# Kernel optimization log

Hardware: AMD Instinct MI355X
Metric: run time of the kernel (lower is better)

Reference implementation:

```python
import jax, jax.numpy as jnp
import numpy as np

N_NODES = 100000
N_EDGES = 800000
N_LAYERS = 6
GATE_TYPES = 29
H = 256        # hidden dim
INTER = 256    # inter dim
EDGE_F = 3     # (src_idx, dst_idx, reversed) edge features


def setup_inputs() -> dict:
    key = jax.random.key(0)
    ks = jax.random.split(key, 16)
    gate_type = jax.random.randint(ks[0], (N_NODES,), 0, GATE_TYPES)
    src = jax.random.randint(ks[1], (N_EDGES,), 0, N_NODES)
    dst = jax.random.randint(ks[2], (N_EDGES,), 0, N_NODES)
    w = jax.random.uniform(ks[3], (N_EDGES, EDGE_F), dtype=jnp.float32)
    s = 0.05
    emb = jax.random.normal(ks[4], (GATE_TYPES, H), dtype=jnp.float32) * s
    # QConv per layer: linear1 (no bias): [INTER, H+3]; linear2: [H, H+INTER] + bias
    W1 = jax.random.normal(ks[5], (N_LAYERS, INTER, H + EDGE_F), dtype=jnp.float32) * s
    W2 = jax.random.normal(ks[6], (N_LAYERS, H, H + INTER), dtype=jnp.float32) * s
    b2 = jax.random.normal(ks[7], (N_LAYERS, H), dtype=jnp.float32) * s
    # MLP head 256->256->1
    Wh1 = jax.random.normal(ks[8], (H, H), dtype=jnp.float32) * s
    bh1 = jax.random.normal(ks[9], (H,), dtype=jnp.float32) * s
    Wh2 = jax.random.normal(ks[10], (1, H), dtype=jnp.float32) * s
    bh2 = jax.random.normal(ks[11], (1,), dtype=jnp.float32) * s
    return {"gate_type": gate_type, "src": src, "dst": dst, "w": w,
            "emb": emb, "W1": W1, "W2": W2, "b2": b2,
            "Wh1": Wh1, "bh1": bh1, "Wh2": Wh2, "bh2": bh2}


def reference(gate_type, src, dst, w, emb, W1, W2, b2, Wh1, bh1, Wh2, bh2):
    n = gate_type.shape[0]
    h = emb[gate_type]                                   # [N, H]
    deg = jax.ops.segment_sum(jnp.ones((src.shape[0],), h.dtype), dst, num_segments=n)
    inv_deg = (1.0 / jnp.maximum(deg, 1.0))[:, None]      # mean over mailbox; 0-deg nodes -> h_N = 0
    for l in range(W1.shape[0]):
        m = jnp.concatenate([h[src], w], axis=1)          # [E, H+3] gather
        tmp = jax.nn.leaky_relu(m @ W1[l].T, 0.01)        # [E, INTER]
        h_N = jax.ops.segment_sum(tmp, dst, num_segments=n) * inv_deg  # scatter-mean [N, INTER]
        h = jax.nn.relu(jnp.concatenate([h, h_N], axis=1) @ W2[l].T + b2[l])
    x = jax.nn.relu(h @ Wh1.T + bh1)                      # [N, H]
    return x @ Wh2.T + bh2                                # [N, 1]
```

## Files before the change

### kernel.cpp

```cpp
#include <hip/hip_runtime.h>

#define H 256
#define NLAYERS 6
typedef unsigned int uint32;
typedef unsigned short u16;

typedef __bf16 bf16;
typedef bf16 bf16x8 __attribute__((ext_vector_type(8)));
typedef float f32x4 __attribute__((ext_vector_type(4)));
typedef u16 u16x8 __attribute__((ext_vector_type(8)));

__device__ __forceinline__ float bf2f(u16 h) {
    return __uint_as_float(((uint32)h) << 16);
}
__device__ __forceinline__ u16 f2bf(float f) {
    uint32 u = __float_as_uint(f);
    u = u + 0x7FFFu + ((u >> 16) & 1u);
    return (u16)(u >> 16);
}

__device__ __forceinline__ void glds16(const void* src, const char* ldsdst) {
    __builtin_amdgcn_global_load_lds(
        (const __attribute__((address_space(1))) void*)src,
        (__attribute__((address_space(3))) void*)ldsdst, 16, 0, 0);
}


__global__ __launch_bounds__(256)
void count_kernel(const int* __restrict__ dst, int* __restrict__ deg, int E) {
    int e = blockIdx.x * 256 + threadIdx.x;
    if (e < E) atomicAdd(&deg[dst[e]], 1);
}

__global__ __launch_bounds__(256)
void invd_kernel(const int* __restrict__ deg, float* __restrict__ invd, int N) {
    int n = blockIdx.x * 256 + threadIdx.x;
    if (n < N) invd[n] = 1.f / fmaxf((float)deg[n], 1.f);
}

__global__ __launch_bounds__(256)
void scan1_kernel(const int* __restrict__ deg, int* __restrict__ bsum, int N) {
    __shared__ int s[256];
    int t = threadIdx.x;
    int i = blockIdx.x * 256 + t;
    s[t] = (i < N) ? deg[i] : 0;
    __syncthreads();
    for (int off = 128; off; off >>= 1) {
        if (t < off) s[t] += s[t + off];
        __syncthreads();
    }
    if (t == 0) bsum[blockIdx.x] = s[0];
}

__global__ __launch_bounds__(512)
void scan2_kernel(int* __restrict__ bsum, int nb) {
    __shared__ int s[512];
    int t = threadIdx.x;
    int v = (t < nb) ? bsum[t] : 0;
    s[t] = v;
    __syncthreads();
    for (int off = 1; off < 512; off <<= 1) {
        int x = (t >= off) ? s[t - off] : 0;
        __syncthreads();
        s[t] += x;
        __syncthreads();
    }
    if (t < nb) bsum[t] = s[t] - v;
}

__global__ __launch_bounds__(256)
void scan3_kernel(const int* __restrict__ deg, const int* __restrict__ bsum,
                  int* __restrict__ rowptr, int N, int E) {
    __shared__ int s[256];
    int t = threadIdx.x;
    int i = blockIdx.x * 256 + t;
    int v = (i < N) ? deg[i] : 0;
    s[t] = v;
    __syncthreads();
    for (int off = 1; off < 256; off <<= 1) {
        int x = (t >= off) ? s[t - off] : 0;
        __syncthreads();
        s[t] += x;
        __syncthreads();
    }
    if (i < N) rowptr[i] = s[t] - v + bsum[blockIdx.x];
    if (i == 0) rowptr[N] = E;
}

__global__ __launch_bounds__(256)
void scatter_kernel(const int* __restrict__ src, const int* __restrict__ dst,
                    const float* __restrict__ w, const int* __restrict__ rowptr,
                    int* __restrict__ cursor, int* __restrict__ srcS,
                    float* __restrict__ wS, int E) {
    int e = blockIdx.x * 256 + threadIdx.x;
    if (e >= E) return;
    int d = dst[e];
    int p = rowptr[d] + atomicAdd(&cursor[d], 1);
    srcS[p] = src[e];
    float4 wq;
    wq.x = w[(size_t)e * 3 + 0];
    wq.y = w[(size_t)e * 3 + 1];
    wq.z = w[(size_t)e * 3 + 2];
    wq.w = 0.f;
    *(float4*)&wS[(size_t)p * 4] = wq;
}


__global__ __launch_bounds__(256)
void wsplit_kernel(const float* __restrict__ W1, const float* __restrict__ W2,
                   const float* __restrict__ Wh1,
                   u16* __restrict__ W1hi, u16* __restrict__ W1lo,
                   u16* __restrict__ W2hi, u16* __restrict__ W2lo,
                   u16* __restrict__ Wh1hi, u16* __restrict__ Wh1lo)
{
    int i = blockIdx.x * 256 + threadIdx.x;
    float v; u16* ph; u16* pl; int o;
    if (i < 393216) {
        int l = i >> 16, rem = i & 65535, r = rem >> 8, k = rem & 255;
        v = W1[(size_t)l * 66304 + (size_t)r * 259 + k];
        ph = W1hi; pl = W1lo; o = i;
    } else if (i < 1179648) {
        int j = i - 393216;
        v = W2[j];
        ph = W2hi; pl = W2lo; o = j;
    } else if (i < 1245184) {
        int j = i - 1179648;
        v = Wh1[j];
        ph = Wh1hi; pl = Wh1lo; o = j;
    } else return;
    u16 hi = f2bf(v);
    ph[o] = hi;
    pl[o] = f2bf(v - bf2f(hi));
}

__global__ void extract_kernel(const float* __restrict__ W1, float* __restrict__ ccAll)
{
    int l = blockIdx.x;
    int i = threadIdx.x;
    const float* W1l = W1 + (size_t)l * 66304;
    float* cc = ccAll + (size_t)l * 768;
    #pragma unroll
    for (int j = 0; j < 3; ++j)
        cc[j * 256 + i] = W1l[(size_t)i * 259 + 256 + j];
}


__global__ __launch_bounds__(256)
void emb_split_kernel(const int* __restrict__ gt, const float* __restrict__ emb,
                      u16* __restrict__ hHi, u16* __restrict__ hLo, int N) {
    size_t idx = (size_t)blockIdx.x * 256 + threadIdx.x;
    if (idx >= (size_t)N * 256) return;
    int n = (int)(idx >> 8), c = (int)(idx & 255);
    float v = emb[(size_t)gt[n] * 256 + c];
    u16 hi = f2bf(v);
    hHi[idx] = hi;
    hLo[idx] = f2bf(v - bf2f(hi));
}


#define LDS_AHI 0
#define LDS_ALO 4096
#define LDS_WHI 8192
#define LDS_WLO 24576

template<bool MAIN>
__device__ __forceinline__ void do_compute(const char* lds, const int* aoff,
                                           const int* woff, f32x4 (&acc)[4][4]) {
    bf16x8 ah[4], al[4];
    #pragma unroll
    for (int mi = 0; mi < 4; ++mi) {
        ah[mi] = *(const bf16x8*)(lds + LDS_AHI + aoff[mi]);
        if (MAIN) al[mi] = *(const bf16x8*)(lds + LDS_ALO + aoff[mi]);
    }
    #pragma unroll
    for (int nj = 0; nj < 4; ++nj) {
        bf16x8 wh = *(const bf16x8*)(lds + LDS_WHI + woff[nj]);
        bf16x8 wl = *(const bf16x8*)(lds + LDS_WLO + woff[nj]);
        #pragma unroll
        for (int mi = 0; mi < 4; ++mi) {
            acc[mi][nj] = __builtin_amdgcn_mfma_f32_16x16x32_bf16(wh, ah[mi], acc[mi][nj], 0, 0, 0);
            acc[mi][nj] = __builtin_amdgcn_mfma_f32_16x16x32_bf16(wl, ah[mi], acc[mi][nj], 0, 0, 0);
            if (MAIN)
                acc[mi][nj] = __builtin_amdgcn_mfma_f32_16x16x32_bf16(wh, al[mi], acc[mi][nj], 0, 0, 0);
        }
    }
}

template<int KTOT, bool BIASRELU, bool WLO>
__global__ __launch_bounds__(256)
void mfma_gemm_kernel(const u16* __restrict__ Ahi_, const u16* __restrict__ Alo_,
                      const u16* __restrict__ A2_,
                      const u16* __restrict__ Whi_, const u16* __restrict__ Wlo_,
                      const float* __restrict__ bias,
                      u16* __restrict__ Chi, u16* __restrict__ Clo, int M)
{
    __shared__ __align__(128) char lds[40960];
    const int tid = threadIdx.x;
    const int wv = tid >> 6;
    const int lane = tid & 63;
    const int m0 = blockIdx.x * 64;
    const int lrow = lane & 15, koct = lane >> 4;

    int aoff[4], woff[4];
    #pragma unroll
    for (int mi = 0; mi < 4; ++mi) {
        int r = mi * 16 + lrow;
        aoff[mi] = r * 64 + ((koct ^ (r & 3)) << 4);
    }
    #pragma unroll
    for (int nj = 0; nj < 4; ++nj) {
        int r = wv * 64 + nj * 16 + lrow;
        woff[nj] = r * 64 + ((koct ^ (r & 3)) << 4);
    }

    const int arow = tid >> 2;
    const int acs = (tid & 3) ^ (arow & 3);
    const long agrow = (long)((m0 + arow < M) ? (m0 + arow) : (M - 1));
    const char* Asrc_hi = (const char*)Ahi_ + agrow * 512 + acs * 16;
    const char* Asrc_lo = (const char*)Alo_ + agrow * 512 + acs * 16;
    const char* Asrc_2  = (const char*)A2_  + agrow * 512 + acs * 16;

    f32x4 acc[4][4] = {};

    for (int k0 = 0; k0 < 256; k0 += 32) {
        glds16(Asrc_hi + k0 * 2, lds + LDS_AHI + wv * 1024);
        glds16(Asrc_lo + k0 * 2, lds + LDS_ALO + wv * 1024);
        #pragma unroll
        for (int rr = 0; rr < 4; ++rr) {
            int f = rr * 256 + tid;
            int wr = f >> 2;
            int wcs = (f & 3) ^ (wr & 3);
            glds16((const char*)Whi_ + (long)wr * (KTOT * 2) + k0 * 2 + wcs * 16,
                   lds + LDS_WHI + rr * 4096 + wv * 1024);
            glds16((const char*)Wlo_ + (long)wr * (KTOT * 2) + k0 * 2 + wcs * 16,
                   lds + LDS_WLO + rr * 4096 + wv * 1024);
        }
        __syncthreads();
        do_compute<true>(lds, aoff, woff, acc);
        __syncthreads();
    }
    if (KTOT > 256) {
        for (int k0 = 256; k0 < KTOT; k0 += 32) {
            glds16(Asrc_2 + (k0 - 256) * 2, lds + LDS_AHI + wv * 1024);
            #pragma unroll
            for (int rr = 0; rr < 4; ++rr) {
                int f = rr * 256 + tid;
                int wr = f >> 2;
                int wcs = (f & 3) ^ (wr & 3);
                glds16((const char*)Whi_ + (long)wr * (KTOT * 2) + k0 * 2 + wcs * 16,
                       lds + LDS_WHI + rr * 4096 + wv * 1024);
                glds16((const char*)Wlo_ + (long)wr * (KTOT * 2) + k0 * 2 + wcs * 16,
                       lds + LDS_WLO + rr * 4096 + wv * 1024);
            }
            __syncthreads();
            do_compute<false>(lds, aoff, woff, acc);
            __syncthreads();
        }
    }

    float4 bv[4];
    if (BIASRELU) {
        #pragma unroll
        for (int nj = 0; nj < 4; ++nj)
            bv[nj] = *(const float4*)&bias[wv * 64 + nj * 16 + koct * 4];
    }
    #pragma unroll
    for (int mi = 0; mi < 4; ++mi) {
        int row = m0 + mi * 16 + lrow;
        if (row >= M) continue;
        #pragma unroll
        for (int nj = 0; nj < 4; ++nj) {
            f32x4 v = acc[mi][nj];
            if (BIASRELU) {
                v[0] = fmaxf(v[0] + bv[nj].x, 0.f);
                v[1] = fmaxf(v[1] + bv[nj].y, 0.f);
                v[2] = fmaxf(v[2] + bv[nj].z, 0.f);
                v[3] = fmaxf(v[3] + bv[nj].w, 0.f);
            }
            size_t o = (size_t)row * 256 + wv * 64 + nj * 16 + koct * 4;
            ushort4 ohi;
            ohi.x = f2bf(v[0]); ohi.y = f2bf(v[1]);
            ohi.z = f2bf(v[2]); ohi.w = f2bf(v[3]);
            *(ushort4*)&Chi[o] = ohi;
            if (WLO) {
                ushort4 olo;
                olo.x = f2bf(v[0] - bf2f(ohi.x));
                olo.y = f2bf(v[1] - bf2f(ohi.y));
                olo.z = f2bf(v[2] - bf2f(ohi.z));
                olo.w = f2bf(v[3] - bf2f(ohi.w));
                *(ushort4*)&Clo[o] = olo;
            }
        }
    }
}


__global__ __launch_bounds__(256)
void edge_agg_kernel(const int* __restrict__ rowptr, const int* __restrict__ srcS,
                     const float* __restrict__ wS, const u16* __restrict__ T,
                     const float* __restrict__ cc, const float* __restrict__ invd,
                     u16* __restrict__ hN, int N) {
    int n = blockIdx.x * 4 + (threadIdx.x >> 6);
    int lane = threadIdx.x & 63;
    if (n >= N) return;
    const int half = lane >> 5;
    const int c32 = lane & 31;
    const int col0 = c32 * 8;

    float c0[8], c1[8], c2[8];
    #pragma unroll
    for (int j = 0; j < 3; ++j) {
        float4 lo4 = *(const float4*)&cc[j * 256 + col0];
        float4 hi4 = *(const float4*)&cc[j * 256 + col0 + 4];
        float* cj = (j == 0) ? c0 : (j == 1) ? c1 : c2;
        cj[0] = lo4.x; cj[1] = lo4.y; cj[2] = lo4.z; cj[3] = lo4.w;
        cj[4] = hi4.x; cj[5] = hi4.y; cj[6] = hi4.z; cj[7] = hi4.w;
    }

    float acc[8] = {};
    const int e0 = rowptr[n], e1 = rowptr[n + 1];
    int e = e0 + half;
    for (; e + 2 < e1; e += 4) {
        int s0 = srcS[e];
        int s1 = srcS[e + 2];
        float4 wa = *(const float4*)&wS[(size_t)e * 4];
        float4 wb = *(const float4*)&wS[(size_t)(e + 2) * 4];
        u16x8 t0 = *(const u16x8*)&T[(size_t)s0 * 256 + col0];
        u16x8 t1 = *(const u16x8*)&T[(size_t)s1 * 256 + col0];
        #pragma unroll
        for (int q = 0; q < 8; ++q) {
            float x = fmaf(wa.x, c0[q], fmaf(wa.y, c1[q], fmaf(wa.z, c2[q], bf2f(t0[q]))));
            acc[q] += (x > 0.f) ? x : 0.01f * x;
            float y = fmaf(wb.x, c0[q], fmaf(wb.y, c1[q], fmaf(wb.z, c2[q], bf2f(t1[q]))));
            acc[q] += (y > 0.f) ? y : 0.01f * y;
        }
    }
    for (; e < e1; e += 2) {
        int s0 = srcS[e];
        float4 wa = *(const float4*)&wS[(size_t)e * 4];
        u16x8 t0 = *(const u16x8*)&T[(size_t)s0 * 256 + col0];
        #pragma unroll
        for (int q = 0; q < 8; ++q) {
            float x = fmaf(wa.x, c0[q], fmaf(wa.y, c1[q], fmaf(wa.z, c2[q], bf2f(t0[q]))));
            acc[q] += (x > 0.f) ? x : 0.01f * x;
        }
    }
    #pragma unroll
    for (int q = 0; q < 8; ++q) acc[q] += __shfl_xor(acc[q], 32);
    if (half == 0) {
        float sc = invd[n];
        u16x8 o;
        #pragma unroll
        for (int q = 0; q < 8; ++q) o[q] = f2bf(acc[q] * sc);
        *(u16x8*)&hN[(size_t)n * 256 + col0] = o;
    }
}


__global__ __launch_bounds__(256)
void head_out_kernel(const u16* __restrict__ xhi, const u16* __restrict__ xlo,
                     const float* __restrict__ wh2,
                     const float* __restrict__ bh2, float* __restrict__ out, int N) {
    int n = blockIdx.x * 4 + (threadIdx.x >> 6);
    int lane = threadIdx.x & 63;
    if (n >= N) return;
    ushort4 hv = ((const ushort4*)(xhi + (size_t)n * H))[lane];
    ushort4 lv = ((const ushort4*)(xlo + (size_t)n * H))[lane];
    float4 wv = ((const float4*)wh2)[lane];
    float x0 = bf2f(hv.x) + bf2f(lv.x);
    float x1 = bf2f(hv.y) + bf2f(lv.y);
    float x2 = bf2f(hv.z) + bf2f(lv.z);
    float x3 = bf2f(hv.w) + bf2f(lv.w);
    float sum = x0 * wv.x + x1 * wv.y + x2 * wv.z + x3 * wv.w;
    #pragma unroll
    for (int off = 32; off; off >>= 1) sum += __shfl_xor(sum, off);
    if (lane == 0) out[n] = sum + bh2[0];
}


extern "C" void kernel_launch(void* const* d_in, const int* in_sizes, int n_in,
                              void* d_out, int out_size, void* d_ws, size_t ws_size,
                              hipStream_t stream) {
    const int*   gate_type = (const int*)d_in[0];
    const int*   src  = (const int*)d_in[1];
    const int*   dst  = (const int*)d_in[2];
    const float* w    = (const float*)d_in[3];
    const float* emb  = (const float*)d_in[4];
    const float* W1   = (const float*)d_in[5];
    const float* W2   = (const float*)d_in[6];
    const float* b2   = (const float*)d_in[7];
    const float* Wh1  = (const float*)d_in[8];
    const float* bh1  = (const float*)d_in[9];
    const float* Wh2  = (const float*)d_in[10];
    const float* bh2  = (const float*)d_in[11];
    float* out = (float*)d_out;

    const int N = in_sizes[0];
    const int E = in_sizes[1];

    char* p = (char*)d_ws;
    auto alloc = [&](size_t bytes) -> char* {
        char* r = p;
        p += (bytes + 1023) & ~(size_t)1023;
        return r;
    };
    u16*   hHi   = (u16*)  alloc((size_t)N * H * 2);
    u16*   hLo   = (u16*)  alloc((size_t)N * H * 2);
    u16*   tBuf  = (u16*)  alloc((size_t)N * H * 2);
    u16*   hNBuf = (u16*)  alloc((size_t)N * H * 2);
    int*   srcS  = (int*)  alloc((size_t)E * 4);
    float* wS    = (float*)alloc((size_t)E * 4 * 4);
    int*   rowptr= (int*)  alloc((size_t)(N + 1) * 4);
    int*   cursor= (int*)  alloc((size_t)N * 4);
    int*   bsum  = (int*)  alloc(4096);
    float* invd  = (float*)alloc((size_t)N * 4);
    float* ccAll = (float*)alloc(6u * 768 * 4);
    u16*   W1hi  = (u16*)  alloc(6u * 256 * 256 * 2);
    u16*   W1lo  = (u16*)  alloc(6u * 256 * 256 * 2);
    u16*   W2hi  = (u16*)  alloc(6u * 256 * 512 * 2);
    u16*   W2lo  = (u16*)  alloc(6u * 256 * 512 * 2);
    u16*   Wh1hi = (u16*)  alloc(256u * 256 * 2);
    u16*   Wh1lo = (u16*)  alloc(256u * 256 * 2);

    const int nb1 = (N + 255) / 256;

    hipMemsetAsync(cursor, 0, (size_t)N * 4, stream);
    count_kernel<<<(E + 255) / 256, 256, 0, stream>>>(dst, cursor, E);
    invd_kernel<<<nb1, 256, 0, stream>>>(cursor, invd, N);
    scan1_kernel<<<nb1, 256, 0, stream>>>(cursor, bsum, N);
    scan2_kernel<<<1, 512, 0, stream>>>(bsum, nb1);
    scan3_kernel<<<nb1, 256, 0, stream>>>(cursor, bsum, rowptr, N, E);
    hipMemsetAsync(cursor, 0, (size_t)N * 4, stream);
    scatter_kernel<<<(E + 255) / 256, 256, 0, stream>>>(src, dst, w, rowptr, cursor, srcS, wS, E);

    wsplit_kernel<<<4864, 256, 0, stream>>>(W1, W2, Wh1, W1hi, W1lo, W2hi, W2lo, Wh1hi, Wh1lo);
    extract_kernel<<<6, 256, 0, stream>>>(W1, ccAll);
    emb_split_kernel<<<N, 256, 0, stream>>>(gate_type, emb, hHi, hLo, N);

    const int gm = (N + 63) / 64;
    for (int l = 0; l < NLAYERS; ++l) {
        mfma_gemm_kernel<256, false, false><<<gm, 256, 0, stream>>>(
            hHi, hLo, nullptr, W1hi + (size_t)l * 65536, W1lo + (size_t)l * 65536,
            nullptr, tBuf, nullptr, N);
        edge_agg_kernel<<<(N + 3) / 4, 256, 0, stream>>>(
            rowptr, srcS, wS, tBuf, ccAll + (size_t)l * 768, invd, hNBuf, N);
        mfma_gemm_kernel<512, true, true><<<gm, 256, 0, stream>>>(
            hHi, hLo, hNBuf, W2hi + (size_t)l * 131072, W2lo + (size_t)l * 131072,
            b2 + (size_t)l * 256, hHi, hLo, N);
    }
    mfma_gemm_kernel<256, true, true><<<gm, 256, 0, stream>>>(
        hHi, hLo, nullptr, Wh1hi, Wh1lo, bh1, hHi, hLo, N);
    head_out_kernel<<<(N + 3) / 4, 256, 0, stream>>>(hHi, hLo, Wh2, bh2, out, N);
}
```

Before: 1.885 ms.

## Enlarge GEMM tile to 128 rows with 8 waves, unroll edge gather by 4

The MFMA GEMM now processes 128 rows per block with 512 threads arranged as 2 row-halves by 4 column groups. This halves the number of times each weight tile is reloaded into LDS per node, and the weight source pointers are precomputed outside the k-loop. The LDS swizzle is changed to use (row>>1)&3. In the edge aggregation kernel the loop is unrolled to four gathers per iteration to put more loads in flight. The cost is more LDS per block (48KB), a larger block that may lower occupancy, and more register pressure in the edge kernel.

```diff
diff --git a/kernel.cpp b/kernel.cpp
--- a/kernel.cpp
+++ b/kernel.cpp
@@ -159,9 +159,9 @@
 
 
 #define LDS_AHI 0
-#define LDS_ALO 4096
-#define LDS_WHI 8192
-#define LDS_WLO 24576
+#define LDS_ALO 8192
+#define LDS_WHI 16384
+#define LDS_WLO 32768
 
 template<bool MAIN>
 __device__ __forceinline__ void do_compute(const char* lds, const int* aoff,
@@ -187,54 +187,56 @@
 }
 
 template<int KTOT, bool BIASRELU, bool WLO>
-__global__ __launch_bounds__(256)
+__global__ __launch_bounds__(512)
 void mfma_gemm_kernel(const u16* __restrict__ Ahi_, const u16* __restrict__ Alo_,
                       const u16* __restrict__ A2_,
                       const u16* __restrict__ Whi_, const u16* __restrict__ Wlo_,
                       const float* __restrict__ bias,
                       u16* __restrict__ Chi, u16* __restrict__ Clo, int M)
 {
-    __shared__ __align__(128) char lds[40960];
+    __shared__ __align__(128) char lds[49152];
     const int tid = threadIdx.x;
     const int wv = tid >> 6;
     const int lane = tid & 63;
-    const int m0 = blockIdx.x * 64;
+    const int m0 = blockIdx.x * 128;
     const int lrow = lane & 15, koct = lane >> 4;
+    const int rh = wv & 1, cg = wv >> 1;
 
     int aoff[4], woff[4];
     #pragma unroll
     for (int mi = 0; mi < 4; ++mi) {
-        int r = mi * 16 + lrow;
-        aoff[mi] = r * 64 + ((koct ^ (r & 3)) << 4);
+        int r = rh * 64 + mi * 16 + lrow;
+        aoff[mi] = r * 64 + ((koct ^ ((r >> 1) & 3)) << 4);
     }
     #pragma unroll
     for (int nj = 0; nj < 4; ++nj) {
-        int r = wv * 64 + nj * 16 + lrow;
-        woff[nj] = r * 64 + ((koct ^ (r & 3)) << 4);
+        int r = cg * 64 + nj * 16 + lrow;
+        woff[nj] = r * 64 + ((koct ^ ((r >> 1) & 3)) << 4);
     }
 
     const int arow = tid >> 2;
-    const int acs = (tid & 3) ^ (arow & 3);
+    const int achk = (tid & 3) ^ ((arow >> 1) & 3);
     const long agrow = (long)((m0 + arow < M) ? (m0 + arow) : (M - 1));
-    const char* Asrc_hi = (const char*)Ahi_ + agrow * 512 + acs * 16;
-    const char* Asrc_lo = (const char*)Alo_ + agrow * 512 + acs * 16;
-    const char* Asrc_2  = (const char*)A2_  + agrow * 512 + acs * 16;
+    const char* Asrc_hi = (const char*)Ahi_ + agrow * 512 + achk * 16;
+    const char* Asrc_lo = (const char*)Alo_ + agrow * 512 + achk * 16;
+    const char* Asrc_2  = (const char*)A2_  + agrow * 512 + achk * 16;
+
+    int wrow0 = tid >> 2,          wchk0 = (tid & 3) ^ ((wrow0 >> 1) & 3);
+    int wrow1 = (512 + tid) >> 2,  wchk1 = ((512 + tid) & 3) ^ ((wrow1 >> 1) & 3);
+    const char* Wsrc_h0 = (const char*)Whi_ + (long)wrow0 * (KTOT * 2) + wchk0 * 16;
+    const char* Wsrc_h1 = (const char*)Whi_ + (long)wrow1 * (KTOT * 2) + wchk1 * 16;
+    const char* Wsrc_l0 = (const char*)Wlo_ + (long)wrow0 * (KTOT * 2) + wchk0 * 16;
+    const char* Wsrc_l1 = (const char*)Wlo_ + (long)wrow1 * (KTOT * 2) + wchk1 * 16;
 
     f32x4 acc[4][4] = {};
 
     for (int k0 = 0; k0 < 256; k0 += 32) {
         glds16(Asrc_hi + k0 * 2, lds + LDS_AHI + wv * 1024);
         glds16(Asrc_lo + k0 * 2, lds + LDS_ALO + wv * 1024);
-        #pragma unroll
-        for (int rr = 0; rr < 4; ++rr) {
-            int f = rr * 256 + tid;
-            int wr = f >> 2;
-            int wcs = (f & 3) ^ (wr & 3);
-            glds16((const char*)Whi_ + (long)wr * (KTOT * 2) + k0 * 2 + wcs * 16,
-                   lds + LDS_WHI + rr * 4096 + wv * 1024);
-            glds16((const char*)Wlo_ + (long)wr * (KTOT * 2) + k0 * 2 + wcs * 16,
-                   lds + LDS_WLO + rr * 4096 + wv * 1024);
-        }
+        glds16(Wsrc_h0 + k0 * 2, lds + LDS_WHI + wv * 1024);
+        glds16(Wsrc_h1 + k0 * 2, lds + LDS_WHI + 8192 + wv * 1024);
+        glds16(Wsrc_l0 + k0 * 2, lds + LDS_WLO + wv * 1024);
+        glds16(Wsrc_l1 + k0 * 2, lds + LDS_WLO + 8192 + wv * 1024);
         __syncthreads();
         do_compute<true>(lds, aoff, woff, acc);
         __syncthreads();
@@ -242,16 +244,10 @@
     if (KTOT > 256) {
         for (int k0 = 256; k0 < KTOT; k0 += 32) {
             glds16(Asrc_2 + (k0 - 256) * 2, lds + LDS_AHI + wv * 1024);
-            #pragma unroll
-            for (int rr = 0; rr < 4; ++rr) {
-                int f = rr * 256 + tid;
-                int wr = f >> 2;
-                int wcs = (f & 3) ^ (wr & 3);
-                glds16((const char*)Whi_ + (long)wr * (KTOT * 2) + k0 * 2 + wcs * 16,
-                       lds + LDS_WHI + rr * 4096 + wv * 1024);
-                glds16((const char*)Wlo_ + (long)wr * (KTOT * 2) + k0 * 2 + wcs * 16,
-                       lds + LDS_WLO + rr * 4096 + wv * 1024);
-            }
+            glds16(Wsrc_h0 + k0 * 2, lds + LDS_WHI + wv * 1024);
+            glds16(Wsrc_h1 + k0 * 2, lds + LDS_WHI + 8192 + wv * 1024);
+            glds16(Wsrc_l0 + k0 * 2, lds + LDS_WLO + wv * 1024);
+            glds16(Wsrc_l1 + k0 * 2, lds + LDS_WLO + 8192 + wv * 1024);
             __syncthreads();
             do_compute<false>(lds, aoff, woff, acc);
             __syncthreads();
@@ -262,11 +258,11 @@
     if (BIASRELU) {
         #pragma unroll
         for (int nj = 0; nj < 4; ++nj)
-            bv[nj] = *(const float4*)&bias[wv * 64 + nj * 16 + koct * 4];
+            bv[nj] = *(const float4*)&bias[cg * 64 + nj * 16 + koct * 4];
     }
     #pragma unroll
     for (int mi = 0; mi < 4; ++mi) {
-        int row = m0 + mi * 16 + lrow;
+        int row = m0 + rh * 64 + mi * 16 + lrow;
         if (row >= M) continue;
         #pragma unroll
         for (int nj = 0; nj < 4; ++nj) {
@@ -277,7 +273,7 @@
                 v[2] = fmaxf(v[2] + bv[nj].z, 0.f);
                 v[3] = fmaxf(v[3] + bv[nj].w, 0.f);
             }
-            size_t o = (size_t)row * 256 + wv * 64 + nj * 16 + koct * 4;
+            size_t o = (size_t)row * 256 + cg * 64 + nj * 16 + koct * 4;
             ushort4 ohi;
             ohi.x = f2bf(v[0]); ohi.y = f2bf(v[1]);
             ohi.z = f2bf(v[2]); ohi.w = f2bf(v[3]);
@@ -320,19 +316,26 @@
     float acc[8] = {};
     const int e0 = rowptr[n], e1 = rowptr[n + 1];
     int e = e0 + half;
-    for (; e + 2 < e1; e += 4) {
-        int s0 = srcS[e];
-        int s1 = srcS[e + 2];
+    for (; e + 6 < e1; e += 8) {
+        int s0 = srcS[e], s1 = srcS[e + 2], s2 = srcS[e + 4], s3 = srcS[e + 6];
         float4 wa = *(const float4*)&wS[(size_t)e * 4];
         float4 wb = *(const float4*)&wS[(size_t)(e + 2) * 4];
+        float4 wc = *(const float4*)&wS[(size_t)(e + 4) * 4];
+        float4 wd = *(const float4*)&wS[(size_t)(e + 6) * 4];
         u16x8 t0 = *(const u16x8*)&T[(size_t)s0 * 256 + col0];
         u16x8 t1 = *(const u16x8*)&T[(size_t)s1 * 256 + col0];
+        u16x8 t2 = *(const u16x8*)&T[(size_t)s2 * 256 + col0];
+        u16x8 t3 = *(const u16x8*)&T[(size_t)s3 * 256 + col0];
         #pragma unroll
         for (int q = 0; q < 8; ++q) {
-            float x = fmaf(wa.x, c0[q], fmaf(wa.y, c1[q], fmaf(wa.z, c2[q], bf2f(t0[q]))));
-            acc[q] += (x > 0.f) ? x : 0.01f * x;
-            float y = fmaf(wb.x, c0[q], fmaf(wb.y, c1[q], fmaf(wb.z, c2[q], bf2f(t1[q]))));
-            acc[q] += (y > 0.f) ? y : 0.01f * y;
+            float x0 = fmaf(wa.x, c0[q], fmaf(wa.y, c1[q], fmaf(wa.z, c2[q], bf2f(t0[q]))));
+            acc[q] += (x0 > 0.f) ? x0 : 0.01f * x0;
+            float x1 = fmaf(wb.x, c0[q], fmaf(wb.y, c1[q], fmaf(wb.z, c2[q], bf2f(t1[q]))));
+            acc[q] += (x1 > 0.f) ? x1 : 0.01f * x1;
+            float x2 = fmaf(wc.x, c0[q], fmaf(wc.y, c1[q], fmaf(wc.z, c2[q], bf2f(t2[q]))));
+            acc[q] += (x2 > 0.f) ? x2 : 0.01f * x2;
+            float x3 = fmaf(wd.x, c0[q], fmaf(wd.y, c1[q], fmaf(wd.z, c2[q], bf2f(t3[q]))));
+            acc[q] += (x3 > 0.f) ? x3 : 0.01f * x3;
         }
     }
     for (; e < e1; e += 2) {
@@ -437,18 +440,18 @@
     extract_kernel<<<6, 256, 0, stream>>>(W1, ccAll);
     emb_split_kernel<<<N, 256, 0, stream>>>(gate_type, emb, hHi, hLo, N);
 
-    const int gm = (N + 63) / 64;
+    const int gm = (N + 127) / 128;
     for (int l = 0; l < NLAYERS; ++l) {
-        mfma_gemm_kernel<256, false, false><<<gm, 256, 0, stream>>>(
+        mfma_gemm_kernel<256, false, false><<<gm, 512, 0, stream>>>(
             hHi, hLo, nullptr, W1hi + (size_t)l * 65536, W1lo + (size_t)l * 65536,
             nullptr, tBuf, nullptr, N);
         edge_agg_kernel<<<(N + 3) / 4, 256, 0, stream>>>(
             rowptr, srcS, wS, tBuf, ccAll + (size_t)l * 768, invd, hNBuf, N);
-        mfma_gemm_kernel<512, true, true><<<gm, 256, 0, stream>>>(
+        mfma_gemm_kernel<512, true, true><<<gm, 512, 0, stream>>>(
             hHi, hLo, hNBuf, W2hi + (size_t)l * 131072, W2lo + (size_t)l * 131072,
             b2 + (size_t)l * 256, hHi, hLo, N);
     }
-    mfma_gemm_kernel<256, true, true><<<gm, 256, 0, stream>>>(
+    mfma_gemm_kernel<256, true, true><<<gm, 512, 0, stream>>>(
         hHi, hLo, nullptr, Wh1hi, Wh1lo, bh1, hHi, hLo, N);
     head_out_kernel<<<(N + 3) / 4, 256, 0, stream>>>(hHi, hLo, Wh2, bh2, out, N);
 }
```

Result: slower. 2.074 ms (+10.0%).
